# Optimization experiments

Measured on AMD Instinct MI355X. Metric: run time of the kernel, lower is better.

## Reference

```python
import jax, jax.numpy as jnp
import numpy as np

N, E, D, R, H = 50000, 200000, 128, 4, 64

def setup_inputs() -> dict:
    key = jax.random.key(0)
    ks = jax.random.split(key, 12)
    s = 0.02
    return {
        'node_feature': jax.random.normal(ks[0], (N, D), dtype=jnp.float32),
        'edge_src': jax.random.randint(ks[1], (E,), 0, N, dtype=jnp.int32),
        'edge_dst': jax.random.randint(ks[2], (E,), 0, N, dtype=jnp.int32),
        'edge_type': jax.random.randint(ks[3], (E,), 0, R, dtype=jnp.int32),
        'Wr1': s * jax.random.normal(ks[4], (R, D, H), dtype=jnp.float32),
        'br1': jnp.zeros((R, H), dtype=jnp.float32),
        'Wr2': s * jax.random.normal(ks[5], (R, H, H), dtype=jnp.float32),
        'br2': jnp.zeros((R, H), dtype=jnp.float32),
        'Wr3': s * jax.random.normal(ks[6], (R, H, D), dtype=jnp.float32),
        'br3': jnp.zeros((R, D), dtype=jnp.float32),
        'Wn1': s * jax.random.normal(ks[7], ((R + 1) * D, H), dtype=jnp.float32),
        'bn1': jnp.zeros((H,), dtype=jnp.float32),
        'Wn2': s * jax.random.normal(ks[8], (H, H), dtype=jnp.float32),
        'bn2': jnp.zeros((H,), dtype=jnp.float32),
        'Wn3': s * jax.random.normal(ks[9], (H, D), dtype=jnp.float32),
        'bn3': jnp.zeros((D,), dtype=jnp.float32),
    }

def reference(node_feature, edge_src, edge_dst, edge_type,
              Wr1, br1, Wr2, br2, Wr3, br3,
              Wn1, bn1, Wn2, bn2, Wn3, bn3):
    n, d = node_feature.shape
    r = Wr1.shape[0]
    # gather source node features per edge  [E, D]
    x_src = node_feature[edge_src]
    # per-relation message MLP over all edges (masked below): relu hidden layers,
    # linear output, then outer relu as in message_function
    h = jax.nn.relu(jnp.einsum('ed,rdh->reh', x_src, Wr1) + br1[:, None, :])
    h = jax.nn.relu(jnp.einsum('reh,rhk->rek', h, Wr2) + br2[:, None, :])
    msg = jax.nn.relu(jnp.einsum('rek,rkd->red', h, Wr3) + br3[:, None, :])  # [R, E, D]
    # zero out edges not of this relation type (mirrors boolean masking)
    mask = (edge_type[None, :] == jnp.arange(r, dtype=edge_type.dtype)[:, None])
    msg = msg * mask[:, :, None].astype(msg.dtype)
    # scatter-sum messages into destination node slots  [R, N, D]
    agg = jax.vmap(lambda m: jax.ops.segment_sum(m, edge_dst, num_segments=n))(msg)
    # node_enc_input: [relu(node_feature), agg_0, ..., agg_{R-1}]  -> [N, (R+1)*D]
    node_in = jnp.concatenate(
        [jax.nn.relu(node_feature), agg.transpose(1, 0, 2).reshape(n, r * d)], axis=1)
    # node updater MLP
    h = jax.nn.relu(node_in @ Wn1 + bn1)
    h = jax.nn.relu(h @ Wn2 + bn2)
    return h @ Wn3 + bn3
```

## Files before the change

### kernel.cpp

```cpp
#include <hip/hip_runtime.h>

#define DD 128
#define HH 64
#define RR 4
#define NT 256
#define NNT 512
#define DGRID 512
#define DPART 128

typedef __attribute__((ext_vector_type(8))) __bf16 bf16x8;
typedef __attribute__((ext_vector_type(4))) float f32x4;

#define SK128 136
#define SK64  72
#define ABLK  2176

#define O_W1  0
#define O_W2  8704
#define O_W3  13312
#define O_WP  22528
#define O_ACT 31232
#define DSMEM_ELEMS 39936
#define N_W1  0
#define N_W2  8704
#define N_W3  13312
#define N_ACT 22528
#define NSMEM_ELEMS 39936

#define W1T_OFF 0
#define W2T_OFF 32768
#define W3T_OFF 49152
#define WPT_OFF 81920
#define WN1_OFF 114688
#define WN2_OFF 122880
#define WN3_OFF 126976
#define WT_TOTAL 135168

#define MFMA(a, b, c) __builtin_amdgcn_mfma_f32_16x16x32_bf16(a, b, c, 0, 0, 0)

template<int ROWS, int COLS, int STRIDE, int BLK>
__device__ __forceinline__ void stageRM(const __bf16* __restrict__ g, __bf16* s, int tid) {
    constexpr int CH = COLS / 8;
    constexpr int TOT = ROWS * CH;
    #pragma unroll
    for (int i = tid; i < TOT; i += BLK) {
        const int row = i / CH, c8 = i % CH;
        *(bf16x8*)(s + row * STRIDE + c8 * 8) = *(const bf16x8*)(g + row * COLS + c8 * 8);
    }
}

__global__ void k_prep_hist(const float* __restrict__ Wr1, const float* __restrict__ Wr2,
                            const float* __restrict__ Wr3, const float* __restrict__ Wn1,
                            const float* __restrict__ Wn2, const float* __restrict__ Wn3,
                            __bf16* __restrict__ wt,
                            const int* __restrict__ ed, int* __restrict__ dstCnt, int E) {
    int i = blockIdx.x * blockDim.x + threadIdx.x;
    if (i < E) atomicAdd(&dstCnt[ed[i]], 1);
    if (i < 32768) {
        int r = i >> 13, k = (i >> 6) & 127, n = i & 63;
        wt[W1T_OFF + r * 8192 + n * 128 + k] = (__bf16)Wr1[i];
    } else if (i < 49152) {
        int j = i - 32768; int r = j >> 12, k = (j >> 6) & 63, n = j & 63;
        wt[W2T_OFF + r * 4096 + n * 64 + k] = (__bf16)Wr2[j];
    } else if (i < 81920) {
        int j = i - 49152; int r = j >> 13, k = (j >> 7) & 63, n = j & 127;
        wt[W3T_OFF + r * 8192 + n * 64 + k] = (__bf16)Wr3[j];
    } else if (i < 122880) {
        int j = i - 81920; int row = j >> 6, n = j & 63;
        int s = row >> 7, k = row & 127;
        float v = Wn1[j];
        if (s == 0) wt[WN1_OFF + n * 128 + k] = (__bf16)v;
        else        wt[WPT_OFF + (s - 1) * 8192 + n * 128 + k] = (__bf16)v;
    } else if (i < 126976) {
        int j = i - 122880; int k = j >> 6, n = j & 63;
        wt[WN2_OFF + n * 64 + k] = (__bf16)Wn2[j];
    } else if (i < WT_TOTAL) {
        int j = i - 126976; int k = j >> 7, n = j & 127;
        wt[WN3_OFF + n * 64 + k] = (__bf16)Wn3[j];
    }
}

__global__ void k_bsum(const int* __restrict__ dstCnt, int* __restrict__ blkSum, int Nn) {
    int b = blockIdx.x, t = threadIdx.x;
    int g = b * 1024 + t * 4;
    int s = 0;
    if (g + 3 < Nn) { int4 v = *(const int4*)(dstCnt + g); s = v.x + v.y + v.z + v.w; }
    else { for (int k = 0; k < 4; k++) if (g + k < Nn) s += dstCnt[g + k]; }
    for (int off = 32; off > 0; off >>= 1) s += __shfl_down(s, off);
    __shared__ int ws[4];
    if ((t & 63) == 0) ws[t >> 6] = s;
    __syncthreads();
    if (t == 0) blkSum[b] = ws[0] + ws[1] + ws[2] + ws[3];
}

__global__ void k_mid(const int* __restrict__ blkSum, int* __restrict__ blkOff,
                      int* __restrict__ rowStart, int NB, int Nn, int E) {
    int lane = threadIdx.x;
    int s = (lane < NB) ? blkSum[lane] : 0;
    int sc = s;
    #pragma unroll
    for (int off = 1; off < 64; off <<= 1) { int u = __shfl_up(sc, off); if (lane >= off) sc += u; }
    if (lane < NB) blkOff[lane] = sc - s;
    if (lane == 0) rowStart[Nn] = E;
}

__global__ void k_wout(const int* __restrict__ dstCnt, const int* __restrict__ blkOff,
                       int* __restrict__ rowStart, int* __restrict__ dstCursor, int Nn) {
    int b = blockIdx.x, t = threadIdx.x;
    int g = b * 1024 + t * 4;
    int4 v = {0, 0, 0, 0};
    bool full = (g + 3 < Nn);
    if (full) v = *(const int4*)(dstCnt + g);
    else {
        if (g     < Nn) v.x = dstCnt[g];
        if (g + 1 < Nn) v.y = dstCnt[g + 1];
        if (g + 2 < Nn) v.z = dstCnt[g + 2];
    }
    int s = v.x + v.y + v.z + v.w;
    int lane = t & 63, wv = t >> 6;
    int sc = s;
    #pragma unroll
    for (int off = 1; off < 64; off <<= 1) { int u = __shfl_up(sc, off); if (lane >= off) sc += u; }
    __shared__ int wsum[4];
    if (lane == 63) wsum[wv] = sc;
    __syncthreads();
    int wadd = 0;
    for (int i = 0; i < wv; i++) wadd += wsum[i];
    int e0 = blkOff[b] + wadd + sc - s;
    int4 rs; rs.x = e0; rs.y = e0 + v.x; rs.z = rs.y + v.y; rs.w = rs.z + v.z;
    if (full) { *(int4*)(rowStart + g) = rs; *(int4*)(dstCursor + g) = rs; }
    else {
        int a[4] = {rs.x, rs.y, rs.z, rs.w};
        for (int k = 0; k < 4; k++) if (g + k < Nn) { rowStart[g + k] = a[k]; dstCursor[g + k] = a[k]; }
    }
}

__global__ void k_place(const int* __restrict__ et, const int* __restrict__ ed,
                        const int* __restrict__ es, int* __restrict__ dstCursor,
                        int* __restrict__ csrKey, int E, int Nn) {
    int i = blockIdx.x * blockDim.x + threadIdx.x;
    if (i < E) {
        int sl = atomicAdd(&dstCursor[ed[i]], 1);
        csrKey[sl] = et[i] * Nn + es[i];
    }
}

__global__ __launch_bounds__(NT, 2) void k_dense(
    const float* __restrict__ nf,
    const float* __restrict__ br1, const float* __restrict__ br2, const float* __restrict__ br3,
    const __bf16* __restrict__ wt, __bf16* __restrict__ ca, int Nn)
{
    extern __shared__ __bf16 smem[];
    const int r    = blockIdx.x & 3;
    const int part = blockIdx.x >> 2;
    const int tid  = threadIdx.x;
    const int w = tid >> 6;
    const int lane = tid & 63;
    const int ln = lane & 15, qd = lane >> 4;
    const int m0 = w << 4;
    __bf16* act = smem + O_ACT + w * ABLK;

    stageRM<64, 128, SK128, NT>(wt + W1T_OFF + r * 8192, smem + O_W1, tid);
    stageRM<64,  64, SK64 , NT>(wt + W2T_OFF + r * 4096, smem + O_W2, tid);
    stageRM<128, 64, SK64 , NT>(wt + W3T_OFF + r * 8192, smem + O_W3, tid);
    stageRM<64, 128, SK128, NT>(wt + WPT_OFF + r * 8192, smem + O_WP, tid);

    float bv1[4], bv2[4], bv3[8];
    #pragma unroll
    for (int nt = 0; nt < 4; nt++) {
        bv1[nt] = br1[r * HH + nt * 16 + ln];
        bv2[nt] = br2[r * HH + nt * 16 + ln];
    }
    #pragma unroll
    for (int nt = 0; nt < 8; nt++) bv3[nt] = br3[r * DD + nt * 16 + ln];

    const int T = (Nn + 63) >> 6;
    const int mx = tid >> 2, qx = tid & 3;
    __bf16* xr = act + (mx & 15) * SK128 + 32 * qx;

    float4 xv[8];
    int t = part;
    if (t < T) {
        const int node = min(t * 64 + mx, Nn - 1);
        const float4* rp = (const float4*)(nf + (size_t)node * DD) + 8 * qx;
        #pragma unroll
        for (int j = 0; j < 8; j++) xv[j] = rp[j];
    }
    __syncthreads();

    for (; t < T; t += DPART) {
        const int nb0 = t * 64;

        #pragma unroll
        for (int jj = 0; jj < 4; jj++) {
            float4 v0 = xv[2 * jj], v1 = xv[2 * jj + 1];
            bf16x8 p;
            p[0] = (__bf16)v0.x; p[1] = (__bf16)v0.y; p[2] = (__bf16)v0.z; p[3] = (__bf16)v0.w;
            p[4] = (__bf16)v1.x; p[5] = (__bf16)v1.y; p[6] = (__bf16)v1.z; p[7] = (__bf16)v1.w;
            *(bf16x8*)(xr + 8 * jj) = p;
        }
        bf16x8 ax[4];
        #pragma unroll
        for (int i = 0; i < 4; i++)
            ax[i] = *(const bf16x8*)(act + ln * SK128 + i * 32 + 8 * qd);

        const int tn = t + DPART;
        if (tn < T) {
            const int node = min(tn * 64 + mx, Nn - 1);
            const float4* rp = (const float4*)(nf + (size_t)node * DD) + 8 * qx;
            #pragma unroll
            for (int j = 0; j < 8; j++) xv[j] = rp[j];
        }

        {
            f32x4 c[4] = {};
            #pragma unroll
            for (int kk = 0; kk < 4; kk++)
                #pragma unroll
                for (int nt = 0; nt < 4; nt++) {
                    bf16x8 b = *(const bf16x8*)(smem + O_W1 + (nt * 16 + ln) * SK128 + kk * 32 + 8 * qd);
                    c[nt] = MFMA(ax[kk], b, c[nt]);
                }
            #pragma unroll
            for (int nt = 0; nt < 4; nt++)
                #pragma unroll
                for (int rg = 0; rg < 4; rg++) {
                    float v = c[nt][rg] + bv1[nt];
                    act[(qd * 4 + rg) * SK64 + nt * 16 + ln] = (__bf16)fmaxf(v, 0.f);
                }
        }
        {
            bf16x8 a0 = *(const bf16x8*)(act + ln * SK64 + 0 + 8 * qd);
            bf16x8 a1 = *(const bf16x8*)(act + ln * SK64 + 32 + 8 * qd);
            f32x4 c[4] = {};
            #pragma unroll
            for (int nt = 0; nt < 4; nt++) {
                bf16x8 b0 = *(const bf16x8*)(smem + O_W2 + (nt * 16 + ln) * SK64 + 0 + 8 * qd);
                bf16x8 b1 = *(const bf16x8*)(smem + O_W2 + (nt * 16 + ln) * SK64 + 32 + 8 * qd);
                c[nt] = MFMA(a0, b0, c[nt]);
                c[nt] = MFMA(a1, b1, c[nt]);
            }
            #pragma unroll
            for (int nt = 0; nt < 4; nt++)
                #pragma unroll
                for (int rg = 0; rg < 4; rg++) {
                    float v = c[nt][rg] + bv2[nt];
                    act[(qd * 4 + rg) * SK64 + nt * 16 + ln] = (__bf16)fmaxf(v, 0.f);
                }
        }
        {
            bf16x8 a0 = *(const bf16x8*)(act + ln * SK64 + 0 + 8 * qd);
            bf16x8 a1 = *(const bf16x8*)(act + ln * SK64 + 32 + 8 * qd);
            f32x4 c[8];
            #pragma unroll
            for (int nt = 0; nt < 8; nt++) {
                bf16x8 b0 = *(const bf16x8*)(smem + O_W3 + (nt * 16 + ln) * SK64 + 0 + 8 * qd);
                bf16x8 b1 = *(const bf16x8*)(smem + O_W3 + (nt * 16 + ln) * SK64 + 32 + 8 * qd);
                f32x4 acc = {};
                acc = MFMA(a0, b0, acc);
                acc = MFMA(a1, b1, acc);
                c[nt] = acc;
            }
            #pragma unroll
            for (int nt = 0; nt < 8; nt++)
                #pragma unroll
                for (int rg = 0; rg < 4; rg++) {
                    float v = c[nt][rg] + bv3[nt];
                    act[(qd * 4 + rg) * SK128 + nt * 16 + ln] = (__bf16)fmaxf(v, 0.f);
                }
        }
        {
            bf16x8 am[4];
            #pragma unroll
            for (int i = 0; i < 4; i++)
                am[i] = *(const bf16x8*)(act + ln * SK128 + i * 32 + 8 * qd);
            f32x4 c[4] = {};
            #pragma unroll
            for (int kk = 0; kk < 4; kk++)
                #pragma unroll
                for (int nt = 0; nt < 4; nt++) {
                    bf16x8 b = *(const bf16x8*)(smem + O_WP + (nt * 16 + ln) * SK128 + kk * 32 + 8 * qd);
                    c[nt] = MFMA(am[kk], b, c[nt]);
                }
            #pragma unroll
            for (int rg = 0; rg < 4; rg++) {
                const int node = nb0 + m0 + qd * 4 + rg;
                if (node < Nn) {
                    __bf16* cp = ca + ((size_t)r * Nn + node) * HH;
                    #pragma unroll
                    for (int nt = 0; nt < 4; nt++)
                        cp[nt * 16 + ln] = (__bf16)c[nt][rg];
                }
            }
        }
    }
}

__global__ __launch_bounds__(NNT, 4) void k_node(
    const float* __restrict__ nf,
    const float* __restrict__ bn1, const float* __restrict__ bn2, const float* __restrict__ bn3,
    const __bf16* __restrict__ wt, const __bf16* __restrict__ ca,
    const int* __restrict__ rowStart, const int* __restrict__ csrKey,
    float* __restrict__ out, int Nn)
{
    extern __shared__ __bf16 smem[];
    const int nb0 = blockIdx.x * 128;
    const int tid = threadIdx.x;
    const int w = tid >> 6;
    const int lane = tid & 63;
    const int ln = lane & 15, qd = lane >> 4;
    const int m0 = w << 4;
    __bf16* act = smem + N_ACT + w * ABLK;

    stageRM<64, 128, SK128, NNT>(wt + WN1_OFF, smem + N_W1, tid);
    stageRM<64,  64, SK64 , NNT>(wt + WN2_OFF, smem + N_W2, tid);
    stageRM<128, 64, SK64 , NNT>(wt + WN3_OFF, smem + N_W3, tid);
    {
        const int m = tid >> 2, q = tid & 3;
        const int node = min(nb0 + m, Nn - 1);
        const float4* rp = (const float4*)(nf + (size_t)node * DD) + 8 * q;
        __bf16* xr = act + (m & 15) * SK128 + 32 * q;
        #pragma unroll
        for (int jj = 0; jj < 4; jj++) {
            float4 v0 = rp[2 * jj], v1 = rp[2 * jj + 1];
            bf16x8 p;
            p[0] = (__bf16)fmaxf(v0.x, 0.f); p[1] = (__bf16)fmaxf(v0.y, 0.f);
            p[2] = (__bf16)fmaxf(v0.z, 0.f); p[3] = (__bf16)fmaxf(v0.w, 0.f);
            p[4] = (__bf16)fmaxf(v1.x, 0.f); p[5] = (__bf16)fmaxf(v1.y, 0.f);
            p[6] = (__bf16)fmaxf(v1.z, 0.f); p[7] = (__bf16)fmaxf(v1.w, 0.f);
            *(bf16x8*)(xr + 8 * jj) = p;
        }
    }
    bf16x8 ax[4];
    #pragma unroll
    for (int i = 0; i < 4; i++)
        ax[i] = *(const bf16x8*)(act + ln * SK128 + i * 32 + 8 * qd);

    float bv1[4], bv2[4], bv3[8];
    #pragma unroll
    for (int nt = 0; nt < 4; nt++) { bv1[nt] = bn1[nt * 16 + ln]; bv2[nt] = bn2[nt * 16 + ln]; }
    #pragma unroll
    for (int nt = 0; nt < 8; nt++) bv3[nt] = bn3[nt * 16 + ln];

    float agg[4][4] = {};
    #pragma unroll
    for (int rg = 0; rg < 4; rg++) {
        const int node = nb0 + m0 + qd * 4 + rg;
        if (node < Nn) {
            const int s0 = rowStart[node], s1 = rowStart[node + 1];
            for (int s = s0; s < s1; s++) {
                const int key = csrKey[s];
                const __bf16* cp = ca + (size_t)key * HH + ln;
                agg[rg][0] += (float)cp[0];
                agg[rg][1] += (float)cp[16];
                agg[rg][2] += (float)cp[32];
                agg[rg][3] += (float)cp[48];
            }
        }
    }
    __syncthreads();

    {
        f32x4 c[4] = {};
        #pragma unroll
        for (int kk = 0; kk < 4; kk++)
            #pragma unroll
            for (int nt = 0; nt < 4; nt++) {
                bf16x8 b = *(const bf16x8*)(smem + N_W1 + (nt * 16 + ln) * SK128 + kk * 32 + 8 * qd);
                c[nt] = MFMA(ax[kk], b, c[nt]);
            }
        #pragma unroll
        for (int nt = 0; nt < 4; nt++)
            #pragma unroll
            for (int rg = 0; rg < 4; rg++) {
                float v = c[nt][rg] + bv1[nt] + agg[rg][nt];
                act[(qd * 4 + rg) * SK64 + nt * 16 + ln] = (__bf16)fmaxf(v, 0.f);
            }
    }
    {
        bf16x8 a0 = *(const bf16x8*)(act + ln * SK64 + 0 + 8 * qd);
        bf16x8 a1 = *(const bf16x8*)(act + ln * SK64 + 32 + 8 * qd);
        f32x4 c[4] = {};
        #pragma unroll
        for (int nt = 0; nt < 4; nt++) {
            bf16x8 b0 = *(const bf16x8*)(smem + N_W2 + (nt * 16 + ln) * SK64 + 0 + 8 * qd);
            bf16x8 b1 = *(const bf16x8*)(smem + N_W2 + (nt * 16 + ln) * SK64 + 32 + 8 * qd);
            c[nt] = MFMA(a0, b0, c[nt]);
            c[nt] = MFMA(a1, b1, c[nt]);
        }
        #pragma unroll
        for (int nt = 0; nt < 4; nt++)
            #pragma unroll
            for (int rg = 0; rg < 4; rg++) {
                float v = c[nt][rg] + bv2[nt];
                act[(qd * 4 + rg) * SK64 + nt * 16 + ln] = (__bf16)fmaxf(v, 0.f);
            }
    }
    {
        bf16x8 a0 = *(const bf16x8*)(act + ln * SK64 + 0 + 8 * qd);
        bf16x8 a1 = *(const bf16x8*)(act + ln * SK64 + 32 + 8 * qd);
        f32x4 c[8];
        #pragma unroll
        for (int nt = 0; nt < 8; nt++) {
            bf16x8 b0 = *(const bf16x8*)(smem + N_W3 + (nt * 16 + ln) * SK64 + 0 + 8 * qd);
            bf16x8 b1 = *(const bf16x8*)(smem + N_W3 + (nt * 16 + ln) * SK64 + 32 + 8 * qd);
            f32x4 acc = {};
            acc = MFMA(a0, b0, acc);
            acc = MFMA(a1, b1, acc);
            c[nt] = acc;
        }
        #pragma unroll
        for (int rg = 0; rg < 4; rg++) {
            const int node = nb0 + m0 + qd * 4 + rg;
            if (node < Nn) {
                float* op = out + (size_t)node * DD;
                #pragma unroll
                for (int nt = 0; nt < 8; nt++)
                    op[nt * 16 + ln] = c[nt][rg] + bv3[nt];
            }
        }
    }
}

extern "C" void kernel_launch(void* const* d_in, const int* in_sizes, int n_in,
                              void* d_out, int out_size, void* d_ws, size_t ws_size,
                              hipStream_t stream) {
    const float* nf  = (const float*)d_in[0];
    const int*   es  = (const int*)d_in[1];
    const int*   ed  = (const int*)d_in[2];
    const int*   et  = (const int*)d_in[3];
    const float* Wr1 = (const float*)d_in[4];
    const float* br1 = (const float*)d_in[5];
    const float* Wr2 = (const float*)d_in[6];
    const float* br2 = (const float*)d_in[7];
    const float* Wr3 = (const float*)d_in[8];
    const float* br3 = (const float*)d_in[9];
    const float* Wn1 = (const float*)d_in[10];
    const float* bn1 = (const float*)d_in[11];
    const float* Wn2 = (const float*)d_in[12];
    const float* bn2 = (const float*)d_in[13];
    const float* Wn3 = (const float*)d_in[14];
    const float* bn3 = (const float*)d_in[15];
    float* out = (float*)d_out;

    const int Nn = in_sizes[0] / DD;
    const int E  = in_sizes[1];
    const int NB = (Nn + 1023) / 1024;

    int* p = (int*)d_ws;
    int* dstCnt    = p;                 p += Nn;
    int* dstCursor = p;                 p += Nn;
    int* rowStart  = p;                 p += Nn + 1;
    int* blkSum    = p;                 p += 64;
    int* blkOff    = p;                 p += 64;
    int* csrKey    = p;                 p += E;
    p += ((8 - ((p - (int*)d_ws) & 7)) & 7);
    __bf16* wbf = (__bf16*)p;           p += (WT_TOTAL + 1) / 2;
    __bf16* ca  = (__bf16*)p;

    hipFuncSetAttribute((const void*)k_dense,
                        hipFuncAttributeMaxDynamicSharedMemorySize,
                        DSMEM_ELEMS * (int)sizeof(__bf16));
    hipFuncSetAttribute((const void*)k_node,
                        hipFuncAttributeMaxDynamicSharedMemorySize,
                        NSMEM_ELEMS * (int)sizeof(__bf16));

    hipMemsetAsync((void*)dstCnt, 0, (size_t)Nn * sizeof(int), stream);

    const int nb = (E + NT - 1) / NT;
    k_prep_hist<<<nb, NT, 0, stream>>>(Wr1, Wr2, Wr3, Wn1, Wn2, Wn3, wbf, ed, dstCnt, E);
    k_bsum <<<NB, 256, 0, stream>>>(dstCnt, blkSum, Nn);
    k_mid  <<<1, 64, 0, stream>>>(blkSum, blkOff, rowStart, NB, Nn, E);
    k_wout <<<NB, 256, 0, stream>>>(dstCnt, blkOff, rowStart, dstCursor, Nn);
    k_place<<<nb, NT, 0, stream>>>(et, ed, es, dstCursor, csrKey, E, Nn);

    k_dense<<<DGRID, NT, DSMEM_ELEMS * sizeof(__bf16), stream>>>(nf, br1, br2, br3, wbf, ca, Nn);
    k_node <<<(Nn + 127) / 128, NNT, NSMEM_ELEMS * sizeof(__bf16), stream>>>(
        nf, bn1, bn2, bn3, wbf, ca, rowStart, csrKey, out, Nn);
}
```

Baseline: 188.6 us.

## Interleave per-node hidden layout and batch CSR gathers across four rows

The projected hidden vectors are now stored interleaved per lane, so each lane writes and reads 4 contiguous bf16 values as one 8-byte access instead of four strided 2-byte accesses. The CSR aggregation loop is restructured to walk all four destination rows at once, two edges per row per iteration. This exposes up to eight independent gathers and loads rowStart once per group. The cost is more predicated control flow and extra registers in the node kernel.

```diff
diff --git a/kernel.cpp b/kernel.cpp
--- a/kernel.cpp
+++ b/kernel.cpp
@@ -9,6 +9,7 @@
 #define DPART 128
 
 typedef __attribute__((ext_vector_type(8))) __bf16 bf16x8;
+typedef __attribute__((ext_vector_type(4))) __bf16 bf16x4;
 typedef __attribute__((ext_vector_type(4))) float f32x4;
 
 #define SK128 136
@@ -37,6 +38,7 @@
 #define WT_TOTAL 135168
 
 #define MFMA(a, b, c) __builtin_amdgcn_mfma_f32_16x16x32_bf16(a, b, c, 0, 0, 0)
+
 
 template<int ROWS, int COLS, int STRIDE, int BLK>
 __device__ __forceinline__ void stageRM(const __bf16* __restrict__ g, __bf16* s, int tid) {
@@ -286,10 +288,10 @@
             for (int rg = 0; rg < 4; rg++) {
                 const int node = nb0 + m0 + qd * 4 + rg;
                 if (node < Nn) {
-                    __bf16* cp = ca + ((size_t)r * Nn + node) * HH;
-                    #pragma unroll
-                    for (int nt = 0; nt < 4; nt++)
-                        cp[nt * 16 + ln] = (__bf16)c[nt][rg];
+                    bf16x4 v;
+                    v[0] = (__bf16)c[0][rg]; v[1] = (__bf16)c[1][rg];
+                    v[2] = (__bf16)c[2][rg]; v[3] = (__bf16)c[3][rg];
+                    *(bf16x4*)(ca + ((size_t)r * Nn + node) * HH + ln * 4) = v;
                 }
             }
         }
@@ -343,18 +345,43 @@
     for (int nt = 0; nt < 8; nt++) bv3[nt] = bn3[nt * 16 + ln];
 
     float agg[4][4] = {};
-    #pragma unroll
-    for (int rg = 0; rg < 4; rg++) {
-        const int node = nb0 + m0 + qd * 4 + rg;
-        if (node < Nn) {
-            const int s0 = rowStart[node], s1 = rowStart[node + 1];
-            for (int s = s0; s < s1; s++) {
-                const int key = csrKey[s];
-                const __bf16* cp = ca + (size_t)key * HH + ln;
-                agg[rg][0] += (float)cp[0];
-                agg[rg][1] += (float)cp[16];
-                agg[rg][2] += (float)cp[32];
-                agg[rg][3] += (float)cp[48];
+    {
+        const int base = nb0 + m0 + qd * 4;
+        int rs[5];
+        #pragma unroll
+        for (int j = 0; j < 5; j++) rs[j] = rowStart[min(base + j, Nn)];
+        int cur[4];
+        #pragma unroll
+        for (int rg = 0; rg < 4; rg++) cur[rg] = rs[rg];
+        const __bf16* cab = ca + ln * 4;
+
+        while (true) {
+            int k0[4], k1[4];
+            bool v0[4], v1[4];
+            bool any = false;
+            #pragma unroll
+            for (int rg = 0; rg < 4; rg++) {
+                const int c0 = cur[rg], e1 = rs[rg + 1];
+                v0[rg] = c0 < e1;
+                v1[rg] = c0 + 1 < e1;
+                if (v0[rg]) k0[rg] = csrKey[c0];
+                if (v1[rg]) k1[rg] = csrKey[c0 + 1];
+                cur[rg] = c0 + (v0[rg] ? 1 : 0) + (v1[rg] ? 1 : 0);
+                any |= v0[rg];
+            }
+            if (!any) break;
+            #pragma unroll
+            for (int rg = 0; rg < 4; rg++) {
+                if (v0[rg]) {
+                    const bf16x4 x = *(const bf16x4*)(cab + (size_t)k0[rg] * HH);
+                    agg[rg][0] += (float)x[0]; agg[rg][1] += (float)x[1];
+                    agg[rg][2] += (float)x[2]; agg[rg][3] += (float)x[3];
+                }
+                if (v1[rg]) {
+                    const bf16x4 x = *(const bf16x4*)(cab + (size_t)k1[rg] * HH);
+                    agg[rg][0] += (float)x[0]; agg[rg][1] += (float)x[1];
+                    agg[rg][2] += (float)x[2]; agg[rg][3] += (float)x[3];
+                }
             }
         }
     }
```

Result: faster. 183.4 us (-2.7%).
